# Optimization experiments

Measured on AMD Instinct MI355X. Metric: run time of the kernel, lower is better.

Reference implementation:

```python
import jax, jax.numpy as jnp
import numpy as np

MODES = 2
NUM_HEADS = 8


def spectral_conv2d(x, wr, wi):
    # x: [B, S, C, H, W]; weights: [C, O, MODES, MODES] (real/imag parts)
    B, S, C, H, W = x.shape
    O = wr.shape[1]
    xf = jnp.fft.rfft2(x, axes=(-2, -1))  # [B,S,C,H,W//2+1] complex
    w = wr + 1j * wi
    out_modes = jnp.einsum('bscxy,coxy->bsoxy', xf[..., :MODES, :MODES], w)
    out_ft = jnp.zeros((B, S, O, H, W // 2 + 1), dtype=xf.dtype)
    out_ft = out_ft.at[..., :MODES, :MODES].set(out_modes)
    return jnp.fft.irfft2(out_ft, s=(H, W), axes=(-2, -1))


def log_cpb(cpb_w1, cpb_b1, cpb_w2, n_sub_x, n_sub_y):
    # Swin-v2 style log-spaced continuous position bias over the subdomain grid.
    gx, gy = jnp.meshgrid(jnp.arange(n_sub_x), jnp.arange(n_sub_y), indexing='ij')
    coords = jnp.stack([gx.reshape(-1), gy.reshape(-1)], axis=-1).astype(jnp.float32)  # [S,2]
    rel = coords[:, None, :] - coords[None, :, :]  # [S,S,2]
    rel = jnp.sign(rel) * jnp.log2(1.0 + jnp.abs(rel))
    h = jax.nn.relu(rel @ cpb_w1 + cpb_b1)  # [S,S,E]
    bias = h @ cpb_w2  # [S,S,nh]
    return jnp.transpose(bias, (2, 0, 1))  # [nh,S,S]


def reference(seq, w_qkv_r, w_qkv_i, w_out_r, w_out_i, cpb_w1, cpb_b1, cpb_w2, n_sub_x, n_sub_y):
    B, S, C, H, W = seq.shape
    hd = C // NUM_HEADS
    # spectral QKV projection: [B,S,3C,H,W]
    qkv = spectral_conv2d(seq, w_qkv_r, w_qkv_i)
    # -> [3, B, nh, S, hd, H, W]
    qkv = qkv.reshape(B, S, 3, NUM_HEADS, hd, H, W).transpose(2, 0, 3, 1, 4, 5, 6)
    q, k, v = qkv[0], qkv[1], qkv[2]
    bias = log_cpb(cpb_w1, cpb_b1, cpb_w2, n_sub_x, n_sub_y)  # [nh,S,S]
    # Riemann quadrature weights (uniform midpoint rule on [0,1]^2): 1/(H*W)
    quad_w = 1.0 / (H * W)
    scale = quad_w / np.sqrt(hd).astype(np.float32)
    # L2-inner-product attention scores via quadrature over the function domain
    scores = jnp.einsum('bhidxy,bhjdxy->bhij', q, k) * scale
    attn = jax.nn.softmax(scores + bias[None], axis=-1)  # [B,nh,S,S]
    out = jnp.einsum('bhij,bhjdxy->bhidxy', attn, v)  # [B,nh,S,hd,H,W]
    out = out.transpose(0, 2, 1, 3, 4, 5).reshape(B, S, C, H, W)
    return spectral_conv2d(out, w_out_r, w_out_i)


def setup_inputs() -> dict:
    key = jax.random.key(0)
    ks = jax.random.split(key, 8)
    B, S, C, H, W = 8, 64, 64, 32, 32
    E, NH = 64, NUM_HEADS
    sc = 0.02
    return {
        'seq': jax.random.normal(ks[0], (B, S, C, H, W), dtype=jnp.float32),
        'w_qkv_r': jax.random.normal(ks[1], (C, 3 * C, MODES, MODES), dtype=jnp.float32) * sc,
        'w_qkv_i': jax.random.normal(ks[2], (C, 3 * C, MODES, MODES), dtype=jnp.float32) * sc,
        'w_out_r': jax.random.normal(ks[3], (C, C, MODES, MODES), dtype=jnp.float32) * sc,
        'w_out_i': jax.random.normal(ks[4], (C, C, MODES, MODES), dtype=jnp.float32) * sc,
        'cpb_w1': jax.random.normal(ks[5], (2, E), dtype=jnp.float32) * 0.1,
        'cpb_b1': jnp.zeros((E,), dtype=jnp.float32),
        'cpb_w2': jax.random.normal(ks[6], (E, NH), dtype=jnp.float32) * 0.1,
        'n_sub_x': 8,
        'n_sub_y': 8,
    }
```

## Files before the change

### kernel.cpp

```cpp
#include <hip/hip_runtime.h>


namespace {

constexpr int Bn = 8, Sn = 64, Cn = 64, NHn = 8;
constexpr int ROWS = Bn * Sn;
constexpr int PLANES = ROWS * Cn;
constexpr float PI2_32 = 0.19634954084936207f;

constexpr float SM0 = 0.59460355750136053f;
constexpr float SM1 = 0.42044820762685725f;

constexpr size_t OFF_A    = 0;
constexpr size_t OFF_G    = OFF_A    + (size_t)ROWS * Cn * 8;
constexpr size_t OFF_BIAS = OFF_G    + (size_t)ROWS * 192 * 8;
constexpr size_t OFF_OG   = OFF_BIAS + (size_t)NHn * Sn * Sn;
constexpr size_t OFF_FC   = OFF_OG   + (size_t)ROWS * Cn * 8;

__global__ __launch_bounds__(256) void k_project(const float* __restrict__ seq,
                                                 float* __restrict__ A) {
    __shared__ float2 tab[32];
    __shared__ float part[4][7];
    int tid = threadIdx.x;
    if (tid < 32) {
        float th = PI2_32 * (float)tid;
        tab[tid] = make_float2(cosf(th), sinf(th));
    }
    __syncthreads();
    size_t plane = blockIdx.x;
    float4 x = ((const float4*)(seq + plane * 1024))[tid];
    int p0 = tid << 2;
    int h = p0 >> 5, w0 = p0 & 31;
    float ch = tab[h].x, sh = tab[h].y;
    float xv[4] = {x.x, x.y, x.z, x.w};
    float s0 = 0.f, s3 = 0.f, s4 = 0.f;
#pragma unroll
    for (int k = 0; k < 4; ++k) {
        float cw = tab[w0 + k].x, sw = tab[w0 + k].y;
        s0 += xv[k];
        s3 = fmaf(xv[k], cw, s3);
        s4 = fmaf(xv[k], sw, s4);
    }
#pragma unroll
    for (int off = 1; off <= 4; off <<= 1) {
        s0 += __shfl_xor(s0, off, 64);
        s3 += __shfl_xor(s3, off, 64);
        s4 += __shfl_xor(s4, off, 64);
    }
    float acc[7];
    acc[0] = s0;
    acc[1] = ch * s0;
    acc[2] = sh * s0;
    acc[3] = s3;
    acc[4] = s4;
    acc[5] = ch * s3 - sh * s4;
    acc[6] = sh * s3 + ch * s4;
#pragma unroll
    for (int off = 8; off <= 32; off <<= 1) {
#pragma unroll
        for (int m = 0; m < 7; ++m) acc[m] += __shfl_xor(acc[m], off, 64);
    }
    int wv = tid >> 6, ln = tid & 63;
    if (ln == 0) {
#pragma unroll
        for (int m = 0; m < 7; ++m) part[wv][m] = acc[m];
    }
    __syncthreads();
    if (tid < 7)
        A[plane * 8 + tid] = part[0][tid] + part[1][tid] + part[2][tid] + part[3][tid];
}

template <int O, int R>
__global__ void k_modemix(const float* __restrict__ In, const float* __restrict__ wr,
                          const float* __restrict__ wi, float* __restrict__ Out,
                          float fac0, float fac1, float fac2, float fac3,
                          int qk_scale) {
    __shared__ float As[R][64][8];
    int tid = threadIdx.x;
    int row0 = blockIdx.x * R;
    {
        const float4* src = (const float4*)(In + (size_t)row0 * 512);
        float4* dst = (float4*)&As[0][0][0];
        for (int idx = tid; idx < R * 128; idx += O) dst[idx] = src[idx];
    }
    __syncthreads();
    float acc[R][7];
#pragma unroll
    for (int r = 0; r < R; ++r)
#pragma unroll
        for (int m = 0; m < 7; ++m) acc[r][m] = 0.f;
    int o = tid;
    const float4* wr4p = (const float4*)wr;
    const float4* wi4p = (const float4*)wi;
    for (int c = 0; c < 64; ++c) {
        float4 r4 = wr4p[c * O + o];
        float4 i4 = wi4p[c * O + o];
#pragma unroll
        for (int r = 0; r < R; ++r) {
            const float* a = As[r][c];
            float a0 = a[0], a1 = a[1], a2 = a[2], a3 = a[3], a4 = a[4], a5 = a[5], a6 = a[6];
            acc[r][0] = fmaf(a0, r4.x, acc[r][0]);
            acc[r][1] = fmaf(a1, r4.z, fmaf(a2, i4.z, acc[r][1]));
            acc[r][2] = fmaf(a2, r4.z, fmaf(-a1, i4.z, acc[r][2]));
            acc[r][3] = fmaf(a3, r4.y, fmaf(a4, i4.y, acc[r][3]));
            acc[r][4] = fmaf(a4, r4.y, fmaf(-a3, i4.y, acc[r][4]));
            acc[r][5] = fmaf(a5, r4.w, fmaf(a6, i4.w, acc[r][5]));
            acc[r][6] = fmaf(a6, r4.w, fmaf(-a5, i4.w, acc[r][6]));
        }
    }
    float f[7] = {fac0, fac1, fac1, fac2, fac2, fac3, fac3};
    bool scale_me = (qk_scale != 0) && (o < 128);
#pragma unroll
    for (int r = 0; r < R; ++r) {
#pragma unroll
        for (int m = 0; m < 7; ++m) {
            float v = acc[r][m] * f[m];
            if (scale_me) v *= (m == 0 ? SM0 : SM1);
            Out[(((size_t)(row0 + r)) * O + o) * 8 + m] = v;
        }
    }
}

__global__ __launch_bounds__(256) void k_cpb(const float* __restrict__ w1,
                                             const float* __restrict__ b1,
                                             const float* __restrict__ w2,
                                             float* __restrict__ bias) {
    __shared__ float W1[128], B1[64], W2[512];
    int tid = threadIdx.x;
    if (tid < 128) W1[tid] = w1[tid];
    if (tid < 64) B1[tid] = b1[tid];
    for (int idx = tid; idx < 512; idx += 256) W2[idx] = w2[idx];
    __syncthreads();
    int p = blockIdx.x * 256 + tid;
    int i = p >> 6, j = p & 63;
    float dx = (float)((i >> 3) - (j >> 3));
    float dy = (float)((i & 7) - (j & 7));
    float r0 = copysignf(log2f(1.f + fabsf(dx)), dx);
    float r1 = copysignf(log2f(1.f + fabsf(dy)), dy);
    float out[8] = {0.f, 0.f, 0.f, 0.f, 0.f, 0.f, 0.f, 0.f};
    for (int e = 0; e < 64; ++e) {
        float hv = fmaxf(fmaf(r0, W1[e], fmaf(r1, W1[64 + e], B1[e])), 0.f);
#pragma unroll
        for (int t = 0; t < 8; ++t) out[t] = fmaf(hv, W2[e * 8 + t], out[t]);
    }
#pragma unroll
    for (int t = 0; t < 8; ++t) bias[(t << 12) + p] = out[t];
}

__global__ __launch_bounds__(256) void k_attn(const float* __restrict__ G,
                                              const float* __restrict__ bias,
                                              float* __restrict__ Og) {
    __shared__ float Qt[56][64];
    __shared__ float Kt[56][64];
    __shared__ float Vs[64][60];
    __shared__ float St[64][68];
    __shared__ float rsum[64];
    int tid = threadIdx.x;
    int bh = blockIdx.x, b = bh >> 3, h = bh & 7;

    for (int idx = tid; idx < 3584; idx += 256) {
        int dm = idx >> 6, s = idx & 63;
        int d = dm / 7, m = dm - d * 7;
        size_t base = ((size_t)(b * 64 + s)) * 1536;
        Qt[dm][s] = G[base + (size_t)(h * 8 + d) * 8 + m];
        Kt[dm][s] = G[base + (size_t)(64 + h * 8 + d) * 8 + m];
    }
    for (int idx = tid; idx < 4096; idx += 256) {
        int s = idx >> 6, dm = idx & 63;
        if (dm < 56) {
            int d = dm / 7, m = dm - d * 7;
            Vs[s][dm] = G[((size_t)(b * 64 + s)) * 1536 + (size_t)(128 + h * 8 + d) * 8 + m];
        }
    }
    __syncthreads();

    {
        int ti = tid >> 4, tj = tid & 15;
        int i0 = ti * 4, j0 = tj * 4;
        float acc[4][4] = {};
        for (int dm = 0; dm < 56; ++dm) {
            float4 q4 = *(const float4*)&Qt[dm][i0];
            float4 k4 = *(const float4*)&Kt[dm][j0];
            float qv[4] = {q4.x, q4.y, q4.z, q4.w};
            float kv[4] = {k4.x, k4.y, k4.z, k4.w};
#pragma unroll
            for (int ii = 0; ii < 4; ++ii)
#pragma unroll
                for (int jj = 0; jj < 4; ++jj) acc[ii][jj] = fmaf(qv[ii], kv[jj], acc[ii][jj]);
        }
        const float* bp = bias + (h << 12);
#pragma unroll
        for (int jj = 0; jj < 4; ++jj)
#pragma unroll
            for (int ii = 0; ii < 4; ++ii)
                St[j0 + jj][i0 + ii] = acc[ii][jj] + bp[(i0 + ii) * 64 + (j0 + jj)];
    }
    __syncthreads();

    {
        int i = tid >> 2, part = tid & 3;
        float mx = -1e30f;
#pragma unroll
        for (int jj = 0; jj < 16; ++jj) mx = fmaxf(mx, St[part * 16 + jj][i]);
        mx = fmaxf(mx, __shfl_xor(mx, 1, 64));
        mx = fmaxf(mx, __shfl_xor(mx, 2, 64));
        float sum = 0.f;
#pragma unroll
        for (int jj = 0; jj < 16; ++jj) {
            int j = part * 16 + jj;
            float e = expf(St[j][i] - mx);
            St[j][i] = e;
            sum += e;
        }
        sum += __shfl_xor(sum, 1, 64);
        sum += __shfl_xor(sum, 2, 64);
        if (part == 0) rsum[i] = 1.f / sum;
    }
    __syncthreads();

    {
        int gi = tid >> 4, gd = tid & 15;
        if (gd < 14) {
            int i0 = gi * 4, dm0 = gd * 4;
            float acc[4][4] = {};
            for (int j = 0; j < 64; ++j) {
                float4 a4 = *(const float4*)&St[j][i0];
                float4 v4 = *(const float4*)&Vs[j][dm0];
                float av[4] = {a4.x, a4.y, a4.z, a4.w};
                float vv[4] = {v4.x, v4.y, v4.z, v4.w};
#pragma unroll
                for (int ii = 0; ii < 4; ++ii)
#pragma unroll
                    for (int k = 0; k < 4; ++k) acc[ii][k] = fmaf(av[ii], vv[k], acc[ii][k]);
            }
#pragma unroll
            for (int ii = 0; ii < 4; ++ii) {
                float ri = rsum[i0 + ii];
#pragma unroll
                for (int k = 0; k < 4; ++k) {
                    int dm = dm0 + k, d = dm / 7, m = dm - d * 7;
                    Og[(((size_t)(b * 64 + i0 + ii)) * 64 + h * 8 + d) * 8 + m] = acc[ii][k] * ri;
                }
            }
        }
    }
}

__global__ __launch_bounds__(256) void k_materialize(const float* __restrict__ Fc,
                                                     float* __restrict__ out) {
    __shared__ float2 tab[32];
    int tid = threadIdx.x;
    if (tid < 32) {
        float th = PI2_32 * (float)tid;
        tab[tid] = make_float2(cosf(th), sinf(th));
    }
    __syncthreads();
    size_t plane = blockIdx.x;
    const float* f = Fc + plane * 8;
    float f0 = f[0], f1 = f[1], f2 = f[2], f3 = f[3], f4 = f[4], f5 = f[5], f6 = f[6];
    int p0 = tid << 2, h = p0 >> 5, w0 = p0 & 31;
    float ch = tab[h].x, sh = tab[h].y;
    float t0 = fmaf(f1, ch, fmaf(f2, sh, f0));
    float t1 = fmaf(f5, ch, fmaf(f6, sh, f3));
    float t2 = fmaf(-f5, sh, fmaf(f6, ch, f4));
    float4 o;
    o.x = fmaf(tab[w0 + 0].x, t1, fmaf(tab[w0 + 0].y, t2, t0));
    o.y = fmaf(tab[w0 + 1].x, t1, fmaf(tab[w0 + 1].y, t2, t0));
    o.z = fmaf(tab[w0 + 2].x, t1, fmaf(tab[w0 + 2].y, t2, t0));
    o.w = fmaf(tab[w0 + 3].x, t1, fmaf(tab[w0 + 3].y, t2, t0));
    ((float4*)(out + plane * 1024))[tid] = o;
}

}

extern "C" void kernel_launch(void* const* d_in, const int* in_sizes, int n_in,
                              void* d_out, int out_size, void* d_ws, size_t ws_size,
                              hipStream_t stream) {
    const float* seq     = (const float*)d_in[0];
    const float* w_qkv_r = (const float*)d_in[1];
    const float* w_qkv_i = (const float*)d_in[2];
    const float* w_out_r = (const float*)d_in[3];
    const float* w_out_i = (const float*)d_in[4];
    const float* cpb_w1  = (const float*)d_in[5];
    const float* cpb_b1  = (const float*)d_in[6];
    const float* cpb_w2  = (const float*)d_in[7];

    float* ws   = (float*)d_ws;
    float* A    = ws + OFF_A;
    float* G    = ws + OFF_G;
    float* bias = ws + OFF_BIAS;
    float* Og   = ws + OFF_OG;
    float* Fc   = ws + OFF_FC;
    float* out  = (float*)d_out;

    k_project<<<dim3(PLANES), dim3(256), 0, stream>>>(seq, A);

    k_modemix<192, 4><<<dim3(ROWS / 4), dim3(192), 0, stream>>>(
        A, w_qkv_r, w_qkv_i, G,
        1.f / 1024.f, 1.f / 1024.f, 2.f / 1024.f, 2.f / 1024.f, 1);

    k_cpb<<<dim3(16), dim3(256), 0, stream>>>(cpb_w1, cpb_b1, cpb_w2, bias);

    k_attn<<<dim3(Bn * NHn), dim3(256), 0, stream>>>(G, bias, Og);

    k_modemix<64, 4><<<dim3(ROWS / 4), dim3(64), 0, stream>>>(
        Og, w_out_r, w_out_i, Fc, 1.f, 0.5f, 1.f, 1.f, 0);

    k_materialize<<<dim3(PLANES), dim3(256), 0, stream>>>(Fc, out);
}
```

Before: 351.5 us.

## Process four planes per block in projection and materialize kernels with nontemporal IO

The projection and materialize kernels now handle four planes per block, using nontemporal vector loads and stores. Twiddle factors are computed in registers instead of through a shared-memory table and barrier. The projection reduction is restructured so each lane reduces a single mode coefficient instead of seven. The mode-mix kernels use fewer rows per block, giving more blocks, and the bias kernel is launched first; this cuts launch count and shuffle traffic at the cost of more sin/cos evaluations per thread.

```diff
diff --git a/kernel.cpp b/kernel.cpp
--- a/kernel.cpp
+++ b/kernel.cpp
@@ -2,10 +2,13 @@
 
 
 namespace {
+
+typedef float vf4 __attribute__((ext_vector_type(4)));
 
 constexpr int Bn = 8, Sn = 64, Cn = 64, NHn = 8;
 constexpr int ROWS = Bn * Sn;
 constexpr int PLANES = ROWS * Cn;
+constexpr int NPP = 4;
 constexpr float PI2_32 = 0.19634954084936207f;
 
 constexpr float SM0 = 0.59460355750136053f;
@@ -19,55 +22,59 @@
 
 __global__ __launch_bounds__(256) void k_project(const float* __restrict__ seq,
                                                  float* __restrict__ A) {
-    __shared__ float2 tab[32];
-    __shared__ float part[4][7];
-    int tid = threadIdx.x;
-    if (tid < 32) {
-        float th = PI2_32 * (float)tid;
-        tab[tid] = make_float2(cosf(th), sinf(th));
-    }
-    __syncthreads();
-    size_t plane = blockIdx.x;
-    float4 x = ((const float4*)(seq + plane * 1024))[tid];
-    int p0 = tid << 2;
-    int h = p0 >> 5, w0 = p0 & 31;
-    float ch = tab[h].x, sh = tab[h].y;
-    float xv[4] = {x.x, x.y, x.z, x.w};
-    float s0 = 0.f, s3 = 0.f, s4 = 0.f;
+    __shared__ float part[NPP][4][8];
+    int tid = threadIdx.x;
+    size_t plane0 = (size_t)blockIdx.x * NPP;
+    const vf4* base = (const vf4*)(seq + plane0 * 1024);
+    vf4 x0 = __builtin_nontemporal_load(base + tid);
+    vf4 x1 = __builtin_nontemporal_load(base + 256 + tid);
+    vf4 x2 = __builtin_nontemporal_load(base + 512 + tid);
+    vf4 x3 = __builtin_nontemporal_load(base + 768 + tid);
+
+    int h = tid >> 3;
+    int w0 = (tid << 2) & 31;
+    float ch = cosf(PI2_32 * (float)h), sh = sinf(PI2_32 * (float)h);
+    float cw[4], sw[4];
 #pragma unroll
     for (int k = 0; k < 4; ++k) {
-        float cw = tab[w0 + k].x, sw = tab[w0 + k].y;
-        s0 += xv[k];
-        s3 = fmaf(xv[k], cw, s3);
-        s4 = fmaf(xv[k], sw, s4);
-    }
-#pragma unroll
-    for (int off = 1; off <= 4; off <<= 1) {
-        s0 += __shfl_xor(s0, off, 64);
-        s3 += __shfl_xor(s3, off, 64);
-        s4 += __shfl_xor(s4, off, 64);
-    }
-    float acc[7];
-    acc[0] = s0;
-    acc[1] = ch * s0;
-    acc[2] = sh * s0;
-    acc[3] = s3;
-    acc[4] = s4;
-    acc[5] = ch * s3 - sh * s4;
-    acc[6] = sh * s3 + ch * s4;
-#pragma unroll
-    for (int off = 8; off <= 32; off <<= 1) {
-#pragma unroll
-        for (int m = 0; m < 7; ++m) acc[m] += __shfl_xor(acc[m], off, 64);
-    }
-    int wv = tid >> 6, ln = tid & 63;
-    if (ln == 0) {
-#pragma unroll
-        for (int m = 0; m < 7; ++m) part[wv][m] = acc[m];
-    }
-    __syncthreads();
-    if (tid < 7)
-        A[plane * 8 + tid] = part[0][tid] + part[1][tid] + part[2][tid] + part[3][tid];
+        float a = PI2_32 * (float)(w0 + k);
+        cw[k] = cosf(a);
+        sw[k] = sinf(a);
+    }
+    int c = tid & 7;
+    float wc0 = (c == 0) ? 1.f : (c == 1) ? ch : (c == 2) ? sh : 0.f;
+    float wc3 = (c == 3) ? 1.f : (c == 5) ? ch : (c == 6) ? sh : 0.f;
+    float wc4 = (c == 4) ? 1.f : (c == 5) ? -sh : (c == 6) ? ch : 0.f;
+
+    vf4 xs[NPP] = {x0, x1, x2, x3};
+#pragma unroll
+    for (int p = 0; p < NPP; ++p) {
+        float xv[4] = {xs[p].x, xs[p].y, xs[p].z, xs[p].w};
+        float s0 = 0.f, s3 = 0.f, s4 = 0.f;
+#pragma unroll
+        for (int k = 0; k < 4; ++k) {
+            s0 += xv[k];
+            s3 = fmaf(xv[k], cw[k], s3);
+            s4 = fmaf(xv[k], sw[k], s4);
+        }
+#pragma unroll
+        for (int off = 1; off <= 4; off <<= 1) {
+            s0 += __shfl_xor(s0, off, 64);
+            s3 += __shfl_xor(s3, off, 64);
+            s4 += __shfl_xor(s4, off, 64);
+        }
+        float acc = fmaf(wc0, s0, fmaf(wc3, s3, wc4 * s4));
+#pragma unroll
+        for (int off = 8; off <= 32; off <<= 1) acc += __shfl_xor(acc, off, 64);
+        if ((tid & 63) < 8) part[p][tid >> 6][c] = acc;
+    }
+    __syncthreads();
+    if (tid < NPP * 8) {
+        int p = tid >> 3, cc = tid & 7;
+        if (cc < 7)
+            A[(plane0 + p) * 8 + cc] =
+                part[p][0][cc] + part[p][1][cc] + part[p][2][cc] + part[p][3][cc];
+    }
 }
 
 template <int O, int R>
@@ -248,27 +255,34 @@
 
 __global__ __launch_bounds__(256) void k_materialize(const float* __restrict__ Fc,
                                                      float* __restrict__ out) {
-    __shared__ float2 tab[32];
-    int tid = threadIdx.x;
-    if (tid < 32) {
-        float th = PI2_32 * (float)tid;
-        tab[tid] = make_float2(cosf(th), sinf(th));
-    }
-    __syncthreads();
-    size_t plane = blockIdx.x;
-    const float* f = Fc + plane * 8;
-    float f0 = f[0], f1 = f[1], f2 = f[2], f3 = f[3], f4 = f[4], f5 = f[5], f6 = f[6];
-    int p0 = tid << 2, h = p0 >> 5, w0 = p0 & 31;
-    float ch = tab[h].x, sh = tab[h].y;
-    float t0 = fmaf(f1, ch, fmaf(f2, sh, f0));
-    float t1 = fmaf(f5, ch, fmaf(f6, sh, f3));
-    float t2 = fmaf(-f5, sh, fmaf(f6, ch, f4));
-    float4 o;
-    o.x = fmaf(tab[w0 + 0].x, t1, fmaf(tab[w0 + 0].y, t2, t0));
-    o.y = fmaf(tab[w0 + 1].x, t1, fmaf(tab[w0 + 1].y, t2, t0));
-    o.z = fmaf(tab[w0 + 2].x, t1, fmaf(tab[w0 + 2].y, t2, t0));
-    o.w = fmaf(tab[w0 + 3].x, t1, fmaf(tab[w0 + 3].y, t2, t0));
-    ((float4*)(out + plane * 1024))[tid] = o;
+    __shared__ float fs[NPP][8];
+    int tid = threadIdx.x;
+    size_t plane0 = (size_t)blockIdx.x * NPP;
+    if (tid < NPP * 8) fs[tid >> 3][tid & 7] = Fc[plane0 * 8 + tid];
+    int h = tid >> 3, w0 = (tid << 2) & 31;
+    float ch = cosf(PI2_32 * (float)h), sh = sinf(PI2_32 * (float)h);
+    float cw[4], sw[4];
+#pragma unroll
+    for (int k = 0; k < 4; ++k) {
+        float a = PI2_32 * (float)(w0 + k);
+        cw[k] = cosf(a);
+        sw[k] = sinf(a);
+    }
+    __syncthreads();
+    vf4* ob = (vf4*)(out + plane0 * 1024);
+#pragma unroll
+    for (int p = 0; p < NPP; ++p) {
+        const float* f = fs[p];
+        float t0 = fmaf(f[1], ch, fmaf(f[2], sh, f[0]));
+        float t1 = fmaf(f[5], ch, fmaf(f[6], sh, f[3]));
+        float t2 = fmaf(-f[5], sh, fmaf(f[6], ch, f[4]));
+        vf4 o;
+        o.x = fmaf(cw[0], t1, fmaf(sw[0], t2, t0));
+        o.y = fmaf(cw[1], t1, fmaf(sw[1], t2, t0));
+        o.z = fmaf(cw[2], t1, fmaf(sw[2], t2, t0));
+        o.w = fmaf(cw[3], t1, fmaf(sw[3], t2, t0));
+        __builtin_nontemporal_store(o, ob + p * 256 + tid);
+    }
 }
 
 }
@@ -293,18 +307,18 @@
     float* Fc   = ws + OFF_FC;
     float* out  = (float*)d_out;
 
-    k_project<<<dim3(PLANES), dim3(256), 0, stream>>>(seq, A);
-
-    k_modemix<192, 4><<<dim3(ROWS / 4), dim3(192), 0, stream>>>(
+    k_cpb<<<dim3(16), dim3(256), 0, stream>>>(cpb_w1, cpb_b1, cpb_w2, bias);
+
+    k_project<<<dim3(PLANES / NPP), dim3(256), 0, stream>>>(seq, A);
+
+    k_modemix<192, 2><<<dim3(ROWS / 2), dim3(192), 0, stream>>>(
         A, w_qkv_r, w_qkv_i, G,
         1.f / 1024.f, 1.f / 1024.f, 2.f / 1024.f, 2.f / 1024.f, 1);
 
-    k_cpb<<<dim3(16), dim3(256), 0, stream>>>(cpb_w1, cpb_b1, cpb_w2, bias);
-
     k_attn<<<dim3(Bn * NHn), dim3(256), 0, stream>>>(G, bias, Og);
 
-    k_modemix<64, 4><<<dim3(ROWS / 4), dim3(64), 0, stream>>>(
+    k_modemix<64, 1><<<dim3(ROWS), dim3(64), 0, stream>>>(
         Og, w_out_r, w_out_i, Fc, 1.f, 0.5f, 1.f, 1.f, 0);
 
-    k_materialize<<<dim3(PLANES), dim3(256), 0, stream>>>(Fc, out);
-}
+    k_materialize<<<dim3(PLANES / NPP), dim3(256), 0, stream>>>(Fc, out);
+}
```

Measured after the change: 297.2 us. 15.4% less time.
